# Kernel tuning notes

Measured on AMD Instinct MI355X. Metric: run time of the kernel, lower is better.

## Reference

```python
import jax, jax.numpy as jnp
import numpy as np

B, S, K, D, F, H, L, MLP = 8, 1024, 11, 512, 768, 8, 4, 2048
HD = D // H
LN_EPS = 1e-5
QK_EPS = 1e-6
SCALE = HD ** -0.5
W_STD = 0.02


def _ln(x, g, b):
    m = x.mean(-1, keepdims=True)
    v = ((x - m) ** 2).mean(-1, keepdims=True)
    return (x - m) / jnp.sqrt(v + LN_EPS) * g + b


def _lin(x, w, b):  # torch Linear: y = x @ W.T + b, W is [out, in]
    return jnp.einsum('...i,oi->...o', x, w) + b


def _heads(x):  # [b, t, D] -> [b, H, t, HD]
    b, t, _ = x.shape
    return x.reshape(b, t, H, HD).transpose(0, 2, 1, 3)


def _l2norm(x):  # F.normalize(dim=-1, eps=QK_EPS)
    n = jnp.sqrt((x * x).sum(-1, keepdims=True))
    return x / jnp.maximum(n, QK_EPS)


def _mha(xq, xkv, qw, qb, kw, kb, vw, vb, ow, ob, mask):
    q = _l2norm(_heads(_lin(xq, qw, qb)))
    k = _l2norm(_heads(_lin(xkv, kw, kb)))
    v = _heads(_lin(xkv, vw, vb))
    s = jnp.einsum('bhtd,bhsd->bhts', q, k) * SCALE
    if mask is not None:
        s = jnp.where(mask, jnp.finfo(s.dtype).min, s)
    a = jax.nn.softmax(s, axis=-1)
    c = jnp.einsum('bhts,bhsd->bhtd', a, v)
    c = c.transpose(0, 2, 1, 3).reshape(xq.shape[0], xq.shape[1], D)
    return _lin(c, ow, ob), a


def setup_inputs() -> dict:
    key = jax.random.key(0)
    ks = jax.random.split(key, 16)
    inp = {
        'features': jax.random.normal(ks[0], (B, S, F), jnp.float32),
        'slots': jax.random.normal(ks[1], (B, K, D), jnp.float32),
        'tok_w': jax.random.normal(ks[2], (D, F), jnp.float32) * W_STD,
        'tok_b': jnp.zeros((D,), jnp.float32),
        'slot_g': jnp.ones((D,), jnp.float32),
        'slot_b': jnp.zeros((D,), jnp.float32),
        'ln1_g': jnp.ones((L, D), jnp.float32),
        'ln1_b': jnp.zeros((L, D), jnp.float32),
        'ln2_g': jnp.ones((L, D), jnp.float32),
        'ln2_b': jnp.zeros((L, D), jnp.float32),
        'ln3_g': jnp.ones((L, D), jnp.float32),
        'ln3_b': jnp.zeros((L, D), jnp.float32),
    }
    names = ['sa_qw', 'sa_kw', 'sa_vw', 'sa_ow', 'ca_qw', 'ca_kw', 'ca_vw', 'ca_ow']
    for i, n in enumerate(names):
        inp[n] = jax.random.normal(ks[3 + i], (L, D, D), jnp.float32) * W_STD
        inp[n[:-1] + 'b'] = jnp.zeros((L, D), jnp.float32)
    inp['ffn_w1'] = jax.random.normal(ks[11], (L, MLP, D), jnp.float32) * W_STD
    inp['ffn_b1'] = jnp.zeros((L, MLP), jnp.float32)
    inp['ffn_w2'] = jax.random.normal(ks[12], (L, D, MLP), jnp.float32) * W_STD
    inp['ffn_b2'] = jnp.zeros((L, D), jnp.float32)
    return inp


def reference(features, slots, tok_w, tok_b, slot_g, slot_b,
              ln1_g, ln1_b, sa_qw, sa_qb, sa_kw, sa_kb, sa_vw, sa_vb, sa_ow, sa_ob,
              ln2_g, ln2_b, ca_qw, ca_qb, ca_kw, ca_kb, ca_vw, ca_vb, ca_ow, ca_ob,
              ln3_g, ln3_b, ffn_w1, ffn_b1, ffn_w2, ffn_b2):
    tokens = _lin(features, tok_w, tok_b)            # [B, S, D]
    slots_n = _ln(slots, slot_g, slot_b)             # [B, K, D]
    causal = jnp.triu(jnp.ones((S, S), bool), k=1)[None, None]  # True = masked
    cross_sum = jnp.zeros((B, S, K), tokens.dtype)
    for l in range(L):
        h = _ln(tokens, ln1_g[l], ln1_b[l])
        sa, _ = _mha(h, h, sa_qw[l], sa_qb[l], sa_kw[l], sa_kb[l],
                     sa_vw[l], sa_vb[l], sa_ow[l], sa_ob[l], causal)
        tokens = tokens + sa
        h = _ln(tokens, ln2_g[l], ln2_b[l])
        ca, w = _mha(h, slots_n, ca_qw[l], ca_qb[l], ca_kw[l], ca_kb[l],
                     ca_vw[l], ca_vb[l], ca_ow[l], ca_ob[l], None)
        tokens = tokens + ca
        cross_sum = cross_sum + w.mean(axis=1)       # avg over heads
        h = _ln(tokens, ln3_g[l], ln3_b[l])
        h = jax.nn.gelu(_lin(h, ffn_w1[l], ffn_b1[l]), approximate=False)
        tokens = tokens + _lin(h, ffn_w2[l], ffn_b2[l])
    masks = cross_sum / L                            # [B, S, K] avg over blocks
    return tokens, masks
```

## Files before the change

### kernel.cpp

```cpp
#include <hip/hip_runtime.h>
#include <math.h>

#define DEV __device__ __forceinline__

typedef __attribute__((ext_vector_type(4))) float f32x4;
typedef __attribute__((ext_vector_type(8))) short bf16x8;

DEV ushort f2bf(float x) {
  unsigned u = __float_as_uint(x);
  u = (u + 0x7FFFu + ((u >> 16) & 1u)) >> 16;
  return (ushort)u;
}

DEV float bf2f(ushort u) { return __uint_as_float(((unsigned)u) << 16); }

DEV ushort4 cvt4(float4 f) {
  ushort4 u;
  u.x = f2bf(f.x); u.y = f2bf(f.y); u.z = f2bf(f.z); u.w = f2bf(f.w);
  return u;
}

DEV float gelu_exact(float x) {
  return 0.5f * x * (1.0f + erff(x * 0.70710678118654752f));
}

DEV void async16(const void* g, void* l) {
  __builtin_amdgcn_global_load_lds((const __attribute__((address_space(1))) void*)g,
                                   (__attribute__((address_space(3))) void*)l, 16, 0, 0);
}

__global__ void prep_all(const float* __restrict__ features, const float* __restrict__ tok_w,
                         const float* __restrict__ sa_qw, const float* __restrict__ sa_kw,
                         const float* __restrict__ sa_vw, const float* __restrict__ sa_ow,
                         const float* __restrict__ ca_qw, const float* __restrict__ ca_kw,
                         const float* __restrict__ ca_vw, const float* __restrict__ ca_ow,
                         const float* __restrict__ ffn_w1, const float* __restrict__ ffn_w2,
                         const float* __restrict__ sa_qb, const float* __restrict__ sa_kb,
                         const float* __restrict__ sa_vb, const float* __restrict__ ca_kb,
                         const float* __restrict__ ca_vb,
                         ushort* __restrict__ featbf, ushort* __restrict__ tokwbf,
                         ushort* __restrict__ saowbf, ushort* __restrict__ caqwbf,
                         ushort* __restrict__ caowbf, ushort* __restrict__ w1bf,
                         ushort* __restrict__ w2bf, ushort* __restrict__ qkvwbf,
                         ushort* __restrict__ kvwbf, float* __restrict__ qkvb,
                         float* __restrict__ kvb, float* __restrict__ masks) {
  long i = (long)blockIdx.x * 256 + threadIdx.x;
  if (i < 1572864) { ((ushort4*)featbf)[i] = cvt4(((const float4*)features)[i]); return; }
  i -= 1572864;
  if (i < 98304) { ((ushort4*)tokwbf)[i] = cvt4(((const float4*)tok_w)[i]); return; }
  i -= 98304;
  if (i < 262144) { ((ushort4*)saowbf)[i] = cvt4(((const float4*)sa_ow)[i]); return; }
  i -= 262144;
  if (i < 262144) { ((ushort4*)caqwbf)[i] = cvt4(((const float4*)ca_qw)[i]); return; }
  i -= 262144;
  if (i < 262144) { ((ushort4*)caowbf)[i] = cvt4(((const float4*)ca_ow)[i]); return; }
  i -= 262144;
  if (i < 1048576) { ((ushort4*)w1bf)[i] = cvt4(((const float4*)ffn_w1)[i]); return; }
  i -= 1048576;
  if (i < 1048576) { ((ushort4*)w2bf)[i] = cvt4(((const float4*)ffn_w2)[i]); return; }
  i -= 1048576;
  if (i < 786432) {
    const long o = i * 4;
    const int layer = (int)(o / 786432), r = (int)(o % 786432);
    const int sel = r / 262144, off = r % 262144;
    const float* s = (sel == 0 ? sa_qw : sel == 1 ? sa_kw : sa_vw) + (size_t)layer * 262144 + off;
    ((ushort4*)qkvwbf)[i] = cvt4(*(const float4*)s);
    return;
  }
  i -= 786432;
  if (i < 524288) {
    const long o = i * 4;
    const int layer = (int)(o / 524288), r = (int)(o % 524288);
    const int sel = r / 262144, off = r % 262144;
    const float* s = (sel == 0 ? ca_kw : ca_vw) + (size_t)layer * 262144 + off;
    ((ushort4*)kvwbf)[i] = cvt4(*(const float4*)s);
    return;
  }
  i -= 524288;
  if (i < 1536) {
    const long o = i * 4;
    const int layer = (int)(o / 1536), r = (int)(o % 1536);
    const int sel = r / 512, off = r % 512;
    const float* s = (sel == 0 ? sa_qb : sel == 1 ? sa_kb : sa_vb) + layer * 512 + off;
    ((float4*)qkvb)[i] = *(const float4*)s;
    return;
  }
  i -= 1536;
  if (i < 1024) {
    const long o = i * 4;
    const int layer = (int)(o / 1024), r = (int)(o % 1024);
    const int sel = r / 512, off = r % 512;
    const float* s = (sel == 0 ? ca_kb : ca_vb) + layer * 512 + off;
    ((float4*)kvb)[i] = *(const float4*)s;
    return;
  }
  i -= 1024;
  if (i < 22528) {
    ((float4*)masks)[i] = make_float4(0.f, 0.f, 0.f, 0.f);
  }
}

template <int EPI>
__launch_bounds__(256, 2)
__global__ void gemm_bt(const ushort* __restrict__ A, const ushort* __restrict__ W,
                        const float* __restrict__ bias, float* __restrict__ Yf,
                        ushort* __restrict__ Ybf, int M, int N, int K) {
  __shared__ ushort As[128 * 32];
  __shared__ ushort Bs[128 * 32];
  const int tid  = threadIdx.x;
  const int lane = tid & 63;
  const int wave = tid >> 6;
  const int wr = wave >> 1, wc = wave & 1;
  const int m0 = blockIdx.x * 128, n0 = blockIdx.y * 128;
  const int q = lane >> 4, ln = lane & 15;
  const int srow = lane >> 2;
  const int scol = (lane & 3) * 8;

  f32x4 acc[4][4] = {};

  const ushort* gA = A + (size_t)(m0 + wave * 32 + srow) * K + scol;
  const ushort* gB = W + (size_t)(n0 + wave * 32 + srow) * K + scol;
  ushort* lA = &As[(wave * 32) * 32];
  ushort* lB = &Bs[(wave * 32) * 32];

  for (int k0 = 0; k0 < K; k0 += 32) {
    async16(gA + k0, lA);
    async16(gA + k0 + (size_t)16 * K, lA + 16 * 32);
    async16(gB + k0, lB);
    async16(gB + k0 + (size_t)16 * K, lB + 16 * 32);
    __syncthreads();
    bf16x8 af[4], bfr[4];
#pragma unroll
    for (int t = 0; t < 4; ++t)
      af[t] = *(const bf16x8*)&As[(wr * 64 + t * 16 + ln) * 32 + q * 8];
#pragma unroll
    for (int t = 0; t < 4; ++t)
      bfr[t] = *(const bf16x8*)&Bs[(wc * 64 + t * 16 + ln) * 32 + q * 8];
#pragma unroll
    for (int mt = 0; mt < 4; ++mt)
#pragma unroll
      for (int nt = 0; nt < 4; ++nt)
        acc[mt][nt] = __builtin_amdgcn_mfma_f32_16x16x32_bf16(af[mt], bfr[nt], acc[mt][nt], 0, 0, 0);
    __syncthreads();
  }

  if (EPI >= 4) {
    const int chunk = (n0 + wc * 64) >> 9;
    const bool donorm = (EPI == 5 && chunk == 0) || (EPI == 6 && chunk < 2);
    const bool doscale = (EPI == 6 && chunk == 0);
#pragma unroll
    for (int mt = 0; mt < 4; ++mt) {
      const int gm = m0 + wr * 64 + mt * 16 + q * 4;
      float val[4][4];
#pragma unroll
      for (int nt = 0; nt < 4; ++nt) {
        const float bi = bias[n0 + wc * 64 + nt * 16 + ln];
#pragma unroll
        for (int r = 0; r < 4; ++r) val[nt][r] = acc[mt][nt][r] + bi;
      }
#pragma unroll
      for (int r = 0; r < 4; ++r) {
        float mult = 1.f;
        if (donorm) {
          float ss = val[0][r]*val[0][r] + val[1][r]*val[1][r] +
                     val[2][r]*val[2][r] + val[3][r]*val[3][r];
          ss += __shfl_xor(ss, 1);
          ss += __shfl_xor(ss, 2);
          ss += __shfl_xor(ss, 4);
          ss += __shfl_xor(ss, 8);
          mult = 1.f / fmaxf(sqrtf(ss), 1e-6f);
          if (doscale) mult *= 0.125f;
        }
#pragma unroll
        for (int nt = 0; nt < 4; ++nt) {
          const int gn = n0 + wc * 64 + nt * 16 + ln;
          Ybf[(size_t)(gm + r) * N + gn] = f2bf(val[nt][r] * mult);
        }
      }
    }
  } else {
#pragma unroll
    for (int mt = 0; mt < 4; ++mt) {
      const int gm = m0 + wr * 64 + mt * 16 + q * 4;
#pragma unroll
      for (int nt = 0; nt < 4; ++nt) {
        const int gn = n0 + wc * 64 + nt * 16 + ln;
        const float bi = bias[gn];
#pragma unroll
        for (int r = 0; r < 4; ++r) {
          const float val = acc[mt][nt][r] + bi;
          const size_t idx = (size_t)(gm + r) * N + gn;
          if (EPI == 0)      Yf[idx] = val;
          else if (EPI == 1) Yf[idx] += val;
          else               Ybf[idx] = f2bf(gelu_exact(val));
        }
      }
    }
  }
}

template <int EPI>
__launch_bounds__(256, 4)
__global__ void gemm_bt64(const ushort* __restrict__ A, const ushort* __restrict__ W,
                          const float* __restrict__ bias, float* __restrict__ Yf,
                          ushort* __restrict__ Ybf, int M, int N, int K) {
  __shared__ ushort As[64 * 32];
  __shared__ ushort Bs[64 * 32];
  __shared__ float red[2][32][2];
  const int tid = threadIdx.x, lane = tid & 63, wave = tid >> 6;
  const int wr = wave >> 1, wc = wave & 1;
  const int m0 = blockIdx.x * 64, n0 = blockIdx.y * 64;
  const int q = lane >> 4, ln = lane & 15;

  f32x4 acc[2][2] = {};
  const ushort* gA = A + (size_t)(m0 + wave * 16 + (lane >> 2)) * K + (lane & 3) * 8;
  const ushort* gB = W + (size_t)(n0 + wave * 16 + (lane >> 2)) * K + (lane & 3) * 8;
  ushort* lA = &As[wave * 16 * 32];
  ushort* lB = &Bs[wave * 16 * 32];

  for (int k0 = 0; k0 < K; k0 += 32) {
    async16(gA + k0, lA);
    async16(gB + k0, lB);
    __syncthreads();
    bf16x8 af[2], bfr[2];
#pragma unroll
    for (int t = 0; t < 2; ++t)
      af[t] = *(const bf16x8*)&As[(wr * 32 + t * 16 + ln) * 32 + q * 8];
#pragma unroll
    for (int t = 0; t < 2; ++t)
      bfr[t] = *(const bf16x8*)&Bs[(wc * 32 + t * 16 + ln) * 32 + q * 8];
#pragma unroll
    for (int mt = 0; mt < 2; ++mt)
#pragma unroll
      for (int nt = 0; nt < 2; ++nt)
        acc[mt][nt] = __builtin_amdgcn_mfma_f32_16x16x32_bf16(af[mt], bfr[nt], acc[mt][nt], 0, 0, 0);
    __syncthreads();
  }

  if (EPI == 4) {
    float val[2][2][4];
#pragma unroll
    for (int mt = 0; mt < 2; ++mt)
#pragma unroll
      for (int nt = 0; nt < 2; ++nt) {
        const float bi = bias[n0 + wc * 32 + nt * 16 + ln];
#pragma unroll
        for (int r = 0; r < 4; ++r) val[mt][nt][r] = acc[mt][nt][r] + bi;
      }
#pragma unroll
    for (int mt = 0; mt < 2; ++mt)
#pragma unroll
      for (int r = 0; r < 4; ++r) {
        float ss = val[mt][0][r]*val[mt][0][r] + val[mt][1][r]*val[mt][1][r];
        ss += __shfl_xor(ss, 1);
        ss += __shfl_xor(ss, 2);
        ss += __shfl_xor(ss, 4);
        ss += __shfl_xor(ss, 8);
        if (ln == 0) red[wr][mt * 16 + q * 4 + r][wc] = ss;
      }
    __syncthreads();
#pragma unroll
    for (int mt = 0; mt < 2; ++mt) {
      const int gm = m0 + wr * 32 + mt * 16 + q * 4;
#pragma unroll
      for (int r = 0; r < 4; ++r) {
        const float tot = red[wr][mt * 16 + q * 4 + r][0] + red[wr][mt * 16 + q * 4 + r][1];
        const float inv = 0.125f / fmaxf(sqrtf(tot), 1e-6f);
#pragma unroll
        for (int nt = 0; nt < 2; ++nt) {
          const int gn = n0 + wc * 32 + nt * 16 + ln;
          Ybf[(size_t)(gm + r) * N + gn] = f2bf(val[mt][nt][r] * inv);
        }
      }
    }
  } else {
#pragma unroll
    for (int mt = 0; mt < 2; ++mt) {
      const int gm = m0 + wr * 32 + mt * 16 + q * 4;
#pragma unroll
      for (int nt = 0; nt < 2; ++nt) {
        const int gn = n0 + wc * 32 + nt * 16 + ln;
        const float bi = bias[gn];
#pragma unroll
        for (int r = 0; r < 4; ++r) {
          const float val = acc[mt][nt][r] + bi;
          const size_t idx = (size_t)(gm + r) * N + gn;
          if (EPI == 0) Yf[idx] = val;
          else          Yf[idx] += val;
        }
      }
    }
  }
}

template <int BF>
__launch_bounds__(256)
__global__ void ln512(const float* __restrict__ X, const float* __restrict__ G,
                      const float* __restrict__ Bb, void* __restrict__ Yv, int rows) {
  const int lane = threadIdx.x & 63;
  const int wave = threadIdx.x >> 6;
  const int row = blockIdx.x * 4 + wave;
  if (row >= rows) return;
  const float* x = X + (size_t)row * 512 + lane * 8;
  float4 v0 = *(const float4*)x;
  float4 v1 = *(const float4*)(x + 4);
  float s = v0.x + v0.y + v0.z + v0.w + v1.x + v1.y + v1.z + v1.w;
#pragma unroll
  for (int off = 32; off; off >>= 1) s += __shfl_xor(s, off);
  const float mean = s * (1.f / 512.f);
  float d[8] = {v0.x - mean, v0.y - mean, v0.z - mean, v0.w - mean,
                v1.x - mean, v1.y - mean, v1.z - mean, v1.w - mean};
  float ss = d[0]*d[0] + d[1]*d[1] + d[2]*d[2] + d[3]*d[3] +
             d[4]*d[4] + d[5]*d[5] + d[6]*d[6] + d[7]*d[7];
#pragma unroll
  for (int off = 32; off; off >>= 1) ss += __shfl_xor(ss, off);
  const float rstd = rsqrtf(ss * (1.f / 512.f) + 1e-5f);
  const float* gp = G + lane * 8;
  const float* bp = Bb + lane * 8;
  float4 g0 = *(const float4*)gp, g1 = *(const float4*)(gp + 4);
  float4 b0 = *(const float4*)bp, b1 = *(const float4*)(bp + 4);
  float y[8];
  y[0] = d[0]*rstd*g0.x + b0.x; y[1] = d[1]*rstd*g0.y + b0.y;
  y[2] = d[2]*rstd*g0.z + b0.z; y[3] = d[3]*rstd*g0.w + b0.w;
  y[4] = d[4]*rstd*g1.x + b1.x; y[5] = d[5]*rstd*g1.y + b1.y;
  y[6] = d[6]*rstd*g1.z + b1.z; y[7] = d[7]*rstd*g1.w + b1.w;
  if (BF) {
    ushort* o = (ushort*)Yv + (size_t)row * 512 + lane * 8;
    ushort4 u0, u1;
    u0.x = f2bf(y[0]); u0.y = f2bf(y[1]); u0.z = f2bf(y[2]); u0.w = f2bf(y[3]);
    u1.x = f2bf(y[4]); u1.y = f2bf(y[5]); u1.z = f2bf(y[6]); u1.w = f2bf(y[7]);
    *(ushort4*)o = u0; *(ushort4*)(o + 4) = u1;
  } else {
    float* o = (float*)Yv + (size_t)row * 512 + lane * 8;
    *(float4*)o = make_float4(y[0], y[1], y[2], y[3]);
    *(float4*)(o + 4) = make_float4(y[4], y[5], y[6], y[7]);
  }
}

__launch_bounds__(256, 2)
__global__ void attn_self_mfma(const ushort* __restrict__ QKV, ushort* __restrict__ O) {
  constexpr int LDK = 72;
  __shared__ ushort Ks[64 * LDK];
  __shared__ ushort Vt[64 * LDK];
  __shared__ ushort Ps[4][32 * LDK];
  ushort* Qstage = &Ps[0][0];
  const int bi = blockIdx.x;
  const int half = bi >> 8, j = bi & 255;
  const int qt = half ? 7 - (j >> 5) : (j >> 5);
  const int bh = (half << 5) | (j & 31);
  const int b = bh >> 3, h = bh & 7;
  const size_t base = (size_t)b * 1024 * 1536 + h * 64;
  const int tid = threadIdx.x, lane = tid & 63, wave = tid >> 6;
  const int quad = lane >> 4, ln = lane & 15;

  const int kr = tid >> 2, kc0 = (tid & 3) * 16;
  const ushort* kbase = QKV + base + 512 + (size_t)kr * 1536 + kc0;
  const int vk = (tid & 31) * 2, vd0 = (tid >> 5) * 8;
  const ushort* vbase = QKV + base + 1024 + (size_t)vk * 1536 + vd0;

#pragma unroll
  for (int it = 0; it < 4; ++it) {
    const int idx = tid + 256 * it;
    const int r = idx >> 3, c = (idx & 7) * 8;
    *(uint4*)&Qstage[r * LDK + c] =
        *(const uint4*)(QKV + base + (size_t)(qt * 128 + r) * 1536 + c);
  }
  uint4 kreg0 = *(const uint4*)kbase;
  uint4 kreg1 = *(const uint4*)(kbase + 8);
  uint4 vreg0 = *(const uint4*)vbase;
  uint4 vreg1 = *(const uint4*)(vbase + 1536);
  __syncthreads();
  bf16x8 qf[2][2];
#pragma unroll
  for (int mt = 0; mt < 2; ++mt)
#pragma unroll
    for (int kc = 0; kc < 2; ++kc)
      qf[mt][kc] = *(const bf16x8*)&Qstage[(wave * 32 + mt * 16 + ln) * LDK + kc * 32 + quad * 8];

  float l_r[2][4] = {};
  f32x4 o_acc[2][4] = {};

  const int ktmax = 2 * qt + 1;
  for (int kt = 0; kt <= ktmax; ++kt) {
    __syncthreads();
    *(uint4*)&Ks[kr * LDK + kc0]     = kreg0;
    *(uint4*)&Ks[kr * LDK + kc0 + 8] = kreg1;
    {
      const ushort* ua = (const ushort*)&vreg0;
      const ushort* ub = (const ushort*)&vreg1;
#pragma unroll
      for (int jj = 0; jj < 8; ++jj)
        *(unsigned*)&Vt[(vd0 + jj) * LDK + vk] = (unsigned)ua[jj] | ((unsigned)ub[jj] << 16);
    }
    __syncthreads();
    if (kt < ktmax) {
      const size_t nb = (size_t)(kt + 1) * 64 * 1536;
      kreg0 = *(const uint4*)(kbase + nb);
      kreg1 = *(const uint4*)(kbase + nb + 8);
      vreg0 = *(const uint4*)(vbase + nb);
      vreg1 = *(const uint4*)(vbase + nb + 1536);
    }

    bf16x8 kf[4][2];
#pragma unroll
    for (int kb = 0; kb < 4; ++kb)
#pragma unroll
      for (int kc = 0; kc < 2; ++kc)
        kf[kb][kc] = *(const bf16x8*)&Ks[(kb * 16 + ln) * LDK + kc * 32 + quad * 8];
    f32x4 s[2][4] = {};
#pragma unroll
    for (int mt = 0; mt < 2; ++mt)
#pragma unroll
      for (int kb = 0; kb < 4; ++kb) {
        s[mt][kb] = __builtin_amdgcn_mfma_f32_16x16x32_bf16(qf[mt][0], kf[kb][0], s[mt][kb], 0, 0, 0);
        s[mt][kb] = __builtin_amdgcn_mfma_f32_16x16x32_bf16(qf[mt][1], kf[kb][1], s[mt][kb], 0, 0, 0);
      }

    const bool diag = (kt >= 2 * qt);
#pragma unroll
    for (int mt = 0; mt < 2; ++mt) {
      const int qrow0 = qt * 128 + wave * 32 + mt * 16 + quad * 4;
#pragma unroll
      for (int kb = 0; kb < 4; ++kb) {
        const int kcol = kt * 64 + kb * 16 + ln;
#pragma unroll
        for (int r = 0; r < 4; ++r) {
          float p = __expf(s[mt][kb][r]);
          if (diag && kcol > qrow0 + r) p = 0.f;
          l_r[mt][r] += p;
          Ps[wave][(mt * 16 + quad * 4 + r) * LDK + kb * 16 + ln] = f2bf(p);
        }
      }
    }
    __builtin_amdgcn_wave_barrier();

    bf16x8 pf[2][2];
#pragma unroll
    for (int mt = 0; mt < 2; ++mt)
#pragma unroll
      for (int kc = 0; kc < 2; ++kc)
        pf[mt][kc] = *(const bf16x8*)&Ps[wave][(mt * 16 + ln) * LDK + kc * 32 + quad * 8];
#pragma unroll
    for (int db = 0; db < 4; ++db) {
      bf16x8 vf0 = *(const bf16x8*)&Vt[(db * 16 + ln) * LDK + quad * 8];
      bf16x8 vf1 = *(const bf16x8*)&Vt[(db * 16 + ln) * LDK + 32 + quad * 8];
#pragma unroll
      for (int mt = 0; mt < 2; ++mt) {
        o_acc[mt][db] = __builtin_amdgcn_mfma_f32_16x16x32_bf16(pf[mt][0], vf0, o_acc[mt][db], 0, 0, 0);
        o_acc[mt][db] = __builtin_amdgcn_mfma_f32_16x16x32_bf16(pf[mt][1], vf1, o_acc[mt][db], 0, 0, 0);
      }
    }
  }

  const size_t obase = (size_t)b * 1024 * 512 + h * 64;
#pragma unroll
  for (int mt = 0; mt < 2; ++mt) {
    const int qrow0 = qt * 128 + wave * 32 + mt * 16 + quad * 4;
#pragma unroll
    for (int r = 0; r < 4; ++r) {
      float l = l_r[mt][r];
      l += __shfl_xor(l, 1);
      l += __shfl_xor(l, 2);
      l += __shfl_xor(l, 4);
      l += __shfl_xor(l, 8);
      const float inv = 1.f / l;
      ushort* dst = O + obase + (size_t)(qrow0 + r) * 512;
#pragma unroll
      for (int db = 0; db < 4; ++db)
        dst[db * 16 + ln] = f2bf(o_acc[mt][db][r] * inv);
    }
  }
}

__launch_bounds__(256)
__global__ void attn_cross(const ushort* __restrict__ Q, const ushort* __restrict__ KV,
                           ushort* __restrict__ Obf, float* __restrict__ mask_out) {
  const int rt = blockIdx.x;
  const int bh = blockIdx.y;
  const int b = bh >> 3, h = bh & 7;
  const int tid = threadIdx.x;
  __shared__ float Kcs[11][64];
  __shared__ float Vcs[11][64];
  const size_t base = ((size_t)(b * 1024)) * 512 + h * 64;

  for (int i = tid; i < 704; i += 256) {
    const int k = i >> 6, d = i & 63;
    Kcs[k][d] = bf2f(KV[((size_t)(b * 11 + k)) * 1024 + h * 64 + d]);
    Vcs[k][d] = bf2f(KV[((size_t)(b * 11 + k)) * 1024 + 512 + h * 64 + d]);
  }
  __syncthreads();

  const int g = tid >> 3;
  const int lj = tid & 7;
  const int qrow = rt * 32 + g;
  const int d0 = lj * 8;

  uint4 qv4 = *(const uint4*)(Q + base + (size_t)qrow * 512 + d0);
  const ushort* qu = (const ushort*)&qv4;
  float qv[8];
#pragma unroll
  for (int jj = 0; jj < 8; ++jj) qv[jj] = bf2f(qu[jj]);

  float s[11];
#pragma unroll
  for (int k = 0; k < 11; ++k) {
    float acc = 0.f;
#pragma unroll
    for (int jj = 0; jj < 8; ++jj) acc += qv[jj] * Kcs[k][d0 + jj];
    acc += __shfl_xor(acc, 1);
    acc += __shfl_xor(acc, 2);
    acc += __shfl_xor(acc, 4);
    s[k] = acc;
  }
  float l = 0.f;
#pragma unroll
  for (int k = 0; k < 11; ++k) { s[k] = __expf(s[k]); l += s[k]; }
  const float inv = 1.f / l;
#pragma unroll
  for (int k = 0; k < 11; ++k) s[k] *= inv;

  float* mo = mask_out + ((size_t)(b * 1024 + qrow)) * 11;
  atomicAdd(mo + lj, s[lj] * 0.03125f);
  if (lj < 3) atomicAdd(mo + lj + 8, s[lj + 8] * 0.03125f);

  ushort o8[8];
#pragma unroll
  for (int jj = 0; jj < 8; ++jj) {
    float acc = 0.f;
#pragma unroll
    for (int k = 0; k < 11; ++k) acc += s[k] * Vcs[k][d0 + jj];
    o8[jj] = f2bf(acc);
  }
  *(uint4*)(Obf + base + (size_t)qrow * 512 + d0) = *(const uint4*)o8;
}

extern "C" void kernel_launch(void* const* d_in, const int* in_sizes, int n_in,
                              void* d_out, int out_size, void* d_ws, size_t ws_size,
                              hipStream_t stream) {
  const float* features = (const float*)d_in[0];
  const float* slots    = (const float*)d_in[1];
  const float* tok_w    = (const float*)d_in[2];
  const float* tok_b    = (const float*)d_in[3];
  const float* slot_g   = (const float*)d_in[4];
  const float* slot_b   = (const float*)d_in[5];
  const float* ln1_g    = (const float*)d_in[6];
  const float* ln1_b    = (const float*)d_in[7];
  const float* ln2_g    = (const float*)d_in[8];
  const float* ln2_b    = (const float*)d_in[9];
  const float* ln3_g    = (const float*)d_in[10];
  const float* ln3_b    = (const float*)d_in[11];
  const float* sa_qw = (const float*)d_in[12]; const float* sa_qb = (const float*)d_in[13];
  const float* sa_kw = (const float*)d_in[14]; const float* sa_kb = (const float*)d_in[15];
  const float* sa_vw = (const float*)d_in[16]; const float* sa_vb = (const float*)d_in[17];
  const float* sa_ow = (const float*)d_in[18]; const float* sa_ob = (const float*)d_in[19];
  const float* ca_qw = (const float*)d_in[20]; const float* ca_qb = (const float*)d_in[21];
  const float* ca_kw = (const float*)d_in[22]; const float* ca_kb = (const float*)d_in[23];
  const float* ca_vw = (const float*)d_in[24]; const float* ca_vb = (const float*)d_in[25];
  const float* ca_ow = (const float*)d_in[26]; const float* ca_ob = (const float*)d_in[27];
  const float* ffn_w1 = (const float*)d_in[28]; const float* ffn_b1 = (const float*)d_in[29];
  const float* ffn_w2 = (const float*)d_in[30]; const float* ffn_b2 = (const float*)d_in[31];

  float* tokens = (float*)d_out;
  float* masks  = (float*)d_out + 4194304;

  char* wp = (char*)d_ws;
  size_t off = 0;
  auto carve = [&](size_t bytes) -> void* {
    void* p = wp + off;
    off = (off + bytes + 255) & ~(size_t)255;
    return p;
  };
  ushort* hbf     = (ushort*)carve(8192ull * 512 * 2);
  ushort* qkvbf   = (ushort*)carve(8192ull * 1536 * 2);
  ushort* qbf     = (ushort*)carve(8192ull * 512 * 2);
  ushort* cbf     = (ushort*)carve(8192ull * 512 * 2);
  ushort* hidbf   = (ushort*)carve(8192ull * 2048 * 2);
  ushort* slotsn  = (ushort*)carve(128ull * 512 * 2);
  ushort* kvc     = (ushort*)carve(128ull * 1024 * 2);
  ushort* tokwbf  = (ushort*)carve(512ull * 768 * 2);
  ushort* saowbf  = (ushort*)carve(4ull * 512 * 512 * 2);
  ushort* caqwbf  = (ushort*)carve(4ull * 512 * 512 * 2);
  ushort* caowbf  = (ushort*)carve(4ull * 512 * 512 * 2);
  ushort* w1bf    = (ushort*)carve(4ull * 2048 * 512 * 2);
  ushort* w2bf    = (ushort*)carve(4ull * 512 * 2048 * 2);
  ushort* qkvwbf  = (ushort*)carve(4ull * 1536 * 512 * 2);
  ushort* kvwbf   = (ushort*)carve(4ull * 1024 * 512 * 2);
  float*  qkvb    = (float*)carve(4ull * 1536 * 4);
  float*  kvb     = (float*)carve(4ull * 1024 * 4);
  ushort* featbf  = hidbf;

  prep_all<<<23010, 256, 0, stream>>>(features, tok_w, sa_qw, sa_kw, sa_vw, sa_ow,
                                      ca_qw, ca_kw, ca_vw, ca_ow, ffn_w1, ffn_w2,
                                      sa_qb, sa_kb, sa_vb, ca_kb, ca_vb,
                                      featbf, tokwbf, saowbf, caqwbf, caowbf,
                                      w1bf, w2bf, qkvwbf, kvwbf, qkvb, kvb, masks);

  gemm_bt64<0><<<dim3(128, 8), 256, 0, stream>>>(featbf, tokwbf, tok_b, tokens, (ushort*)nullptr, 8192, 512, 768);
  ln512<1><<<22, 256, 0, stream>>>(slots, slot_g, slot_b, slotsn, 88);

  for (int l = 0; l < 4; ++l) {
    const size_t wD = (size_t)l * 512 * 512;
    const size_t bD = (size_t)l * 512;
    ln512<1><<<2048, 256, 0, stream>>>(tokens, ln1_g + bD, ln1_b + bD, hbf, 8192);
    gemm_bt<6><<<dim3(64, 12), 256, 0, stream>>>(hbf, qkvwbf + (size_t)l * 1536 * 512, qkvb + l * 1536,
                                                 (float*)nullptr, qkvbf, 8192, 1536, 512);
    attn_self_mfma<<<512, 256, 0, stream>>>(qkvbf, cbf);
    gemm_bt64<1><<<dim3(128, 8), 256, 0, stream>>>(cbf, saowbf + wD, sa_ob + bD, tokens, (ushort*)nullptr, 8192, 512, 512);
    ln512<1><<<2048, 256, 0, stream>>>(tokens, ln2_g + bD, ln2_b + bD, hbf, 8192);
    gemm_bt64<4><<<dim3(128, 8), 256, 0, stream>>>(hbf, caqwbf + wD, ca_qb + bD, (float*)nullptr, qbf, 8192, 512, 512);
    gemm_bt<5><<<dim3(1, 8), 256, 0, stream>>>(slotsn, kvwbf + (size_t)l * 1024 * 512, kvb + l * 1024,
                                               (float*)nullptr, kvc, 128, 1024, 512);
    attn_cross<<<dim3(32, 64), 256, 0, stream>>>(qbf, kvc, cbf, masks);
    gemm_bt64<1><<<dim3(128, 8), 256, 0, stream>>>(cbf, caowbf + wD, ca_ob + bD, tokens, (ushort*)nullptr, 8192, 512, 512);
    const size_t wM = (size_t)l * 2048 * 512;
    const size_t bM = (size_t)l * 2048;
    ln512<1><<<2048, 256, 0, stream>>>(tokens, ln3_g + bD, ln3_b + bD, hbf, 8192);
    gemm_bt<2><<<dim3(64, 16), 256, 0, stream>>>(hbf, w1bf + wM, ffn_b1 + bM, (float*)nullptr, hidbf, 8192, 2048, 512);
    gemm_bt64<1><<<dim3(128, 8), 256, 0, stream>>>(hidbf, w2bf + wM, ffn_b2 + bD, tokens, (ushort*)nullptr, 8192, 512, 2048);
  }
}
```

Measured before the change: 1.023 ms.

## Use 128x128 split-K GEMM with atomic accumulation for residual projections

Replaces the 64x64-tile residual-add GEMMs (attention output projections and FFN down projection) with a new 128x128-tile kernel that splits K across two blocks and accumulates into the fp32 residual with atomicAdd. The larger tile raises operand reuse per load, and split-K keeps the grid at 512 blocks. The cost is atomic traffic on the output, with twice as many read-modify-writes to tokens, and a non-deterministic summation order. The new kernel loads each K step without double buffering.

```diff
diff --git a/kernel.cpp b/kernel.cpp
--- a/kernel.cpp
+++ b/kernel.cpp
@@ -199,6 +199,65 @@
   }
 }
 
+__launch_bounds__(256, 2)
+__global__ void gemm_bt_sk(const ushort* __restrict__ A, const ushort* __restrict__ W,
+                           const float* __restrict__ bias, float* __restrict__ Yf,
+                           int M, int N, int K, int Ksplit) {
+  __shared__ ushort As[128 * 32];
+  __shared__ ushort Bs[128 * 32];
+  const int tid  = threadIdx.x;
+  const int lane = tid & 63;
+  const int wave = tid >> 6;
+  const int wr = wave >> 1, wc = wave & 1;
+  const int m0 = blockIdx.x * 128, n0 = blockIdx.y * 128;
+  const int kz = blockIdx.z;
+  const int kbase = kz * Ksplit;
+  const int q = lane >> 4, ln = lane & 15;
+  const int srow = lane >> 2;
+  const int scol = (lane & 3) * 8;
+
+  f32x4 acc[4][4] = {};
+
+  const ushort* gA = A + (size_t)(m0 + wave * 32 + srow) * K + kbase + scol;
+  const ushort* gB = W + (size_t)(n0 + wave * 32 + srow) * K + kbase + scol;
+  ushort* lA = &As[(wave * 32) * 32];
+  ushort* lB = &Bs[(wave * 32) * 32];
+
+  for (int k0 = 0; k0 < Ksplit; k0 += 32) {
+    async16(gA + k0, lA);
+    async16(gA + k0 + (size_t)16 * K, lA + 16 * 32);
+    async16(gB + k0, lB);
+    async16(gB + k0 + (size_t)16 * K, lB + 16 * 32);
+    __syncthreads();
+    bf16x8 af[4], bfr[4];
+#pragma unroll
+    for (int t = 0; t < 4; ++t)
+      af[t] = *(const bf16x8*)&As[(wr * 64 + t * 16 + ln) * 32 + q * 8];
+#pragma unroll
+    for (int t = 0; t < 4; ++t)
+      bfr[t] = *(const bf16x8*)&Bs[(wc * 64 + t * 16 + ln) * 32 + q * 8];
+#pragma unroll
+    for (int mt = 0; mt < 4; ++mt)
+#pragma unroll
+      for (int nt = 0; nt < 4; ++nt)
+        acc[mt][nt] = __builtin_amdgcn_mfma_f32_16x16x32_bf16(af[mt], bfr[nt], acc[mt][nt], 0, 0, 0);
+    __syncthreads();
+  }
+
+#pragma unroll
+  for (int mt = 0; mt < 4; ++mt) {
+    const int gm = m0 + wr * 64 + mt * 16 + q * 4;
+#pragma unroll
+    for (int nt = 0; nt < 4; ++nt) {
+      const int gn = n0 + wc * 64 + nt * 16 + ln;
+      const float bi = (kz == 0) ? bias[gn] : 0.f;
+#pragma unroll
+      for (int r = 0; r < 4; ++r)
+        atomicAdd(&Yf[(size_t)(gm + r) * N + gn], acc[mt][nt][r] + bi);
+    }
+  }
+}
+
 template <int EPI>
 __launch_bounds__(256, 4)
 __global__ void gemm_bt64(const ushort* __restrict__ A, const ushort* __restrict__ W,
@@ -605,17 +664,17 @@
     gemm_bt<6><<<dim3(64, 12), 256, 0, stream>>>(hbf, qkvwbf + (size_t)l * 1536 * 512, qkvb + l * 1536,
                                                  (float*)nullptr, qkvbf, 8192, 1536, 512);
     attn_self_mfma<<<512, 256, 0, stream>>>(qkvbf, cbf);
-    gemm_bt64<1><<<dim3(128, 8), 256, 0, stream>>>(cbf, saowbf + wD, sa_ob + bD, tokens, (ushort*)nullptr, 8192, 512, 512);
+    gemm_bt_sk<<<dim3(64, 4, 2), 256, 0, stream>>>(cbf, saowbf + wD, sa_ob + bD, tokens, 8192, 512, 512, 256);
     ln512<1><<<2048, 256, 0, stream>>>(tokens, ln2_g + bD, ln2_b + bD, hbf, 8192);
     gemm_bt64<4><<<dim3(128, 8), 256, 0, stream>>>(hbf, caqwbf + wD, ca_qb + bD, (float*)nullptr, qbf, 8192, 512, 512);
     gemm_bt<5><<<dim3(1, 8), 256, 0, stream>>>(slotsn, kvwbf + (size_t)l * 1024 * 512, kvb + l * 1024,
                                                (float*)nullptr, kvc, 128, 1024, 512);
     attn_cross<<<dim3(32, 64), 256, 0, stream>>>(qbf, kvc, cbf, masks);
-    gemm_bt64<1><<<dim3(128, 8), 256, 0, stream>>>(cbf, caowbf + wD, ca_ob + bD, tokens, (ushort*)nullptr, 8192, 512, 512);
+    gemm_bt_sk<<<dim3(64, 4, 2), 256, 0, stream>>>(cbf, caowbf + wD, ca_ob + bD, tokens, 8192, 512, 512, 256);
     const size_t wM = (size_t)l * 2048 * 512;
     const size_t bM = (size_t)l * 2048;
     ln512<1><<<2048, 256, 0, stream>>>(tokens, ln3_g + bD, ln3_b + bD, hbf, 8192);
     gemm_bt<2><<<dim3(64, 16), 256, 0, stream>>>(hbf, w1bf + wM, ffn_b1 + bM, (float*)nullptr, hidbf, 8192, 2048, 512);
-    gemm_bt64<1><<<dim3(128, 8), 256, 0, stream>>>(hidbf, w2bf + wM, ffn_b2 + bD, tokens, (ushort*)nullptr, 8192, 512, 2048);
-  }
-}
+    gemm_bt_sk<<<dim3(64, 4, 2), 256, 0, stream>>>(hidbf, w2bf + wM, ffn_b2 + bD, tokens, 8192, 512, 2048, 1024);
+  }
+}
```

Measured after the change: 1.209 ms. +18.2%, slower.
